# Kernel optimization log

Measured on AMD Instinct MI355X. Metric: run time of the kernel, lower is better.

The kernel has to match this reference:

```python
import jax, jax.numpy as jnp
import numpy as np
from jax import lax

# Model dims (match init_kwargs / input_specs)
B, T, N_IN, N_MID, N_OUT = 256, 100, 784, 1024, 10
L_TAU = 0.8  # state decay


def setup_inputs() -> dict:
    key = jax.random.key(0)
    ks = jax.random.split(key, 10)
    x = jax.random.uniform(ks[0], (B, T, N_IN), dtype=jnp.float32)  # input spikes/rates
    y = jax.random.randint(ks[1], (B,), 0, N_OUT, dtype=jnp.int64)

    def lin(k, fan_in, fan_out):
        return jax.random.normal(k, (fan_in, fan_out), dtype=jnp.float32) / np.sqrt(fan_in)

    return {
        "x": x, "y": y,
        "W1": lin(ks[2], N_IN, N_MID),  "b1": jnp.zeros((N_MID,), jnp.float32),
        "W2": lin(ks[3], N_MID, N_MID), "b2": jnp.zeros((N_MID,), jnp.float32),
        "W3": lin(ks[4], N_MID, N_MID), "b3": jnp.zeros((N_MID,), jnp.float32),
        "W4": lin(ks[5], N_MID, N_OUT), "b4": jnp.zeros((N_OUT,), jnp.float32),
    }


def _snu(s, y_prev, x_in, W, b):
    # SNU cell (soft): s_t = relu(W x_t + tau * s_{t-1} * (1 - y_{t-1})); y_t = sigmoid(s_t + b)
    s = jax.nn.relu(x_in @ W + L_TAU * s * (1.0 - y_prev))
    y_out = jax.nn.sigmoid(s + b)
    return s, y_out


def reference(x, y, W1, b1, W2, b2, W3, b3, W4, b4):
    bsz = x.shape[0]
    zeros = lambda n: jnp.zeros((bsz, n), x.dtype)
    carry0 = (zeros(N_MID), zeros(N_MID), zeros(N_MID), zeros(N_MID),
              zeros(N_MID), zeros(N_MID), zeros(N_OUT), zeros(N_OUT))

    def step(carry, x_t):
        s1, y1, s2, y2, s3, y3, s4, y4 = carry
        s1, y1 = _snu(s1, y1, x_t, W1, b1)
        s2, y2 = _snu(s2, y2, y1, W2, b2)
        s3, y3 = _snu(s3, y3, y2, W3, b3)
        s4, y4 = _snu(s4, y4, y3, W4, b4)
        return (s1, y1, s2, y2, s3, y3, s4, y4), y4

    xs = jnp.transpose(x, (1, 0, 2))  # [T, B, n_in]
    _, outs = lax.scan(step, carry0, xs)  # outs: [T, B, n_out]
    # out_rec also stacked the initial zero output; it contributes 0 to the sum
    m = jnp.sum(outs, axis=0)  # [B, n_out]
    logp = jax.nn.log_softmax(m, axis=-1)
    loss = -jnp.mean(jnp.take_along_axis(logp, y[:, None], axis=1))
    return loss, m
```

## Files before the change

kernel.cpp:

```cpp
#include <hip/hip_runtime.h>
#include <hip/hip_bf16.h>


#define BDIM 256
#define TT   100
#define BB   256
#define MM   25600
#define NMID 1024
#define K1   784
#define K1P  896
#define NOUT 10
#define N4P  16
#define L_TAU 0.8f

typedef __attribute__((ext_vector_type(4))) int   int4x;
typedef __attribute__((ext_vector_type(8))) int   int8x;
typedef __attribute__((ext_vector_type(4))) float f32x4;

__device__ __forceinline__ void async_copy16(const void* g, void* l) {
    __builtin_amdgcn_global_load_lds(
        (const __attribute__((address_space(1))) unsigned int*)g,
        (__attribute__((address_space(3))) unsigned int*)l,
        16, 0, 0);
}

__device__ __forceinline__ unsigned short f2bf(float f) {
    __hip_bfloat16 h = __float2bfloat16(f);
    return __builtin_bit_cast(unsigned short, h);
}
__device__ __forceinline__ float bf2f(unsigned short u) {
    return __uint_as_float((unsigned)u << 16);
}

__global__ void convert_x(const float* __restrict__ X, unsigned char* __restrict__ XB) {
    int m = blockIdx.x;
    int b = m & (BB - 1);
    int t = m >> 8;
    int th = threadIdx.x;
    if (th >= K1P / 4) return;
    int pk = 0;
    if (th < K1 / 4) {
        float4 v = *(const float4*)(X + ((long)b * TT + t) * K1 + th * 4);
        pk = __builtin_amdgcn_cvt_pk_fp8_f32(v.x, v.y, 0, false);
        pk = __builtin_amdgcn_cvt_pk_fp8_f32(v.z, v.w, pk, true);
    }
    *(int*)(XB + (long)m * K1P + th * 4) = pk;
}

__device__ __forceinline__ void tc_body(const float* __restrict__ W,
                                        unsigned char* __restrict__ WT,
                                        int K, int N, int Kpad,
                                        int bx, int by, int tidx) {
    __shared__ float tile[32][33];
    int k0 = bx * 32;
    int n0 = by * 32;
    int tx = tidx & 31, ty = tidx >> 5;
    #pragma unroll
    for (int i = 0; i < 4; ++i) {
        int k = k0 + ty + i * 8;
        tile[ty + i * 8][tx] = (k < K) ? W[(long)k * N + n0 + tx] : 0.0f;
    }
    __syncthreads();
    int nl = tidx >> 3, kq = tidx & 7;
    int pk = __builtin_amdgcn_cvt_pk_fp8_f32(tile[kq * 4 + 0][nl], tile[kq * 4 + 1][nl], 0, false);
    pk     = __builtin_amdgcn_cvt_pk_fp8_f32(tile[kq * 4 + 2][nl], tile[kq * 4 + 3][nl], pk, true);
    *(int*)(WT + (long)(n0 + nl) * Kpad + k0 + kq * 4) = pk;
}

__global__ void transpose_convert(const float* __restrict__ W, unsigned char* __restrict__ WT,
                                  int K, int N, int Kpad) {
    tc_body(W, WT, K, N, Kpad, blockIdx.x, blockIdx.y, threadIdx.x);
}

__global__ void transpose_convert2(const float* __restrict__ Wa, unsigned char* __restrict__ Ta,
                                   const float* __restrict__ Wb, unsigned char* __restrict__ Tb) {
    const float* W = blockIdx.z ? Wb : Wa;
    unsigned char* T = blockIdx.z ? Tb : Ta;
    tc_body(W, T, NMID, NMID, NMID, blockIdx.x, blockIdx.y, threadIdx.x);
}

__global__ void convert_w4(const float* __restrict__ W4, unsigned char* __restrict__ W4T) {
    int tid = blockIdx.x * BDIM + threadIdx.x;
    int n = tid >> 8;
    int k4 = (tid & 255) * 4;
    float v0 = 0, v1 = 0, v2 = 0, v3 = 0;
    if (n < NOUT) {
        v0 = W4[(k4 + 0) * NOUT + n];
        v1 = W4[(k4 + 1) * NOUT + n];
        v2 = W4[(k4 + 2) * NOUT + n];
        v3 = W4[(k4 + 3) * NOUT + n];
    }
    int pk = __builtin_amdgcn_cvt_pk_fp8_f32(v0, v1, 0, false);
    pk     = __builtin_amdgcn_cvt_pk_fp8_f32(v2, v3, pk, true);
    *(int*)(W4T + (long)n * NMID + k4) = pk;
}

#define BM 128
#define BN 128
#define BKB 128
#define MSTRIPS (MM / BM)
#define NSTRIPS (NMID / BN)
__global__ __launch_bounds__(256) void gemm_fp8(
    const unsigned char* __restrict__ A,
    const unsigned char* __restrict__ BT,
    __hip_bfloat16* __restrict__ C,
    int Kp)
{
    __shared__ unsigned char As[BM * BKB];
    __shared__ unsigned char Bs[BN * BKB];

    const int tid  = threadIdx.x;
    const int wave = tid >> 6;
    const int lane = tid & 63;

    const int l    = blockIdx.x;
    const int xcd  = l & 7;
    const int p    = l >> 3;
    const int bm   = (xcd * (MSTRIPS / 8) + (p >> 3)) * BM;
    const int bn   = (p & 7) * BN;

    const int wr = (wave >> 1) * 64;
    const int wc = (wave & 1) * 64;

    f32x4 acc[4][4] = {};

    const int srow = tid >> 3;
    const int lch  = tid & 7;
    const int gch  = lch ^ (srow & 7);
    const unsigned char* Aptr = A  + (long)(bm + srow) * Kp + gch * 16;
    const unsigned char* Bptr = BT + (long)(bn + srow) * Kp + gch * 16;

    for (int k0 = 0; k0 < Kp; k0 += BKB) {
        #pragma unroll
        for (int i = 0; i < 4; ++i) {
            async_copy16(Aptr + (long)(i * 32) * Kp + k0, &As[(srow + i * 32) * BKB + lch * 16]);
            async_copy16(Bptr + (long)(i * 32) * Kp + k0, &Bs[(srow + i * 32) * BKB + lch * 16]);
        }
        __syncthreads();

        const int mrow = lane & 15;
        const int g    = lane >> 4;
        int8x af[4], bfr[4];
        #pragma unroll
        for (int i = 0; i < 4; ++i) {
            int row = wr + i * 16 + mrow;
            int r7  = row & 7;
            int4x lo = *(const int4x*)&As[row * BKB + ((2 * g    ) ^ r7) * 16];
            int4x hi = *(const int4x*)&As[row * BKB + ((2 * g + 1) ^ r7) * 16];
            af[i][0] = lo[0]; af[i][1] = lo[1]; af[i][2] = lo[2]; af[i][3] = lo[3];
            af[i][4] = hi[0]; af[i][5] = hi[1]; af[i][6] = hi[2]; af[i][7] = hi[3];
        }
        #pragma unroll
        for (int j = 0; j < 4; ++j) {
            int row = wc + j * 16 + mrow;
            int r7  = row & 7;
            int4x lo = *(const int4x*)&Bs[row * BKB + ((2 * g    ) ^ r7) * 16];
            int4x hi = *(const int4x*)&Bs[row * BKB + ((2 * g + 1) ^ r7) * 16];
            bfr[j][0] = lo[0]; bfr[j][1] = lo[1]; bfr[j][2] = lo[2]; bfr[j][3] = lo[3];
            bfr[j][4] = hi[0]; bfr[j][5] = hi[1]; bfr[j][6] = hi[2]; bfr[j][7] = hi[3];
        }
        #pragma unroll
        for (int i = 0; i < 4; ++i)
            #pragma unroll
            for (int j = 0; j < 4; ++j)
                acc[i][j] = __builtin_amdgcn_mfma_scale_f32_16x16x128_f8f6f4(
                    bfr[j], af[i], acc[i][j],
                    0, 0,
                    0, 0x7F,
                    0, 0x7F);
        __syncthreads();
    }

    const int mcol  = lane & 15;
    const int nrow4 = (lane >> 4) * 4;
    #pragma unroll
    for (int i = 0; i < 4; ++i)
        #pragma unroll
        for (int j = 0; j < 4; ++j) {
            int gm = bm + wr + i * 16 + mcol;
            int gn = bn + wc + j * 16 + nrow4;
            ushort4 pk;
            pk.x = f2bf(acc[i][j][0]);
            pk.y = f2bf(acc[i][j][1]);
            pk.z = f2bf(acc[i][j][2]);
            pk.w = f2bf(acc[i][j][3]);
            *(ushort4*)&C[(long)gm * NMID + gn] = pk;
        }
}

__global__ void snu_recur(const __hip_bfloat16* __restrict__ Z,
                          const float* __restrict__ bias,
                          unsigned char* __restrict__ Y) {
    int idx = blockIdx.x * BDIM + threadIdx.x;
    int n2 = (idx & (NMID / 2 - 1)) * 2;
    int b  = idx >> 9;
    float2 bv = *(const float2*)(bias + n2);
    float s0 = 0.0f, y0 = 0.0f, s1 = 0.0f, y1 = 0.0f;
    const long base = (long)b * NMID + n2;
    const long stride = (long)BB * NMID;
    for (int t0 = 0; t0 < TT; t0 += 4) {
        ushort2 zz[4];
        #pragma unroll
        for (int j = 0; j < 4; ++j)
            zz[j] = *(const ushort2*)(Z + base + (t0 + j) * stride);
        #pragma unroll
        for (int j = 0; j < 4; ++j) {
            float z0 = bf2f(zz[j].x), z1 = bf2f(zz[j].y);
            s0 = fmaxf(fmaf(L_TAU * s0, 1.0f - y0, z0), 0.0f);
            y0 = 1.0f / (1.0f + __expf(-(s0 + bv.x)));
            s1 = fmaxf(fmaf(L_TAU * s1, 1.0f - y1, z1), 0.0f);
            y1 = 1.0f / (1.0f + __expf(-(s1 + bv.y)));
            int pk = __builtin_amdgcn_cvt_pk_fp8_f32(y0, y1, 0, false);
            *(unsigned short*)(Y + base + (t0 + j) * stride) = (unsigned short)pk;
        }
    }
}

__global__ __launch_bounds__(256) void layer4_gemm(const unsigned char* __restrict__ Y3,
                                                   const unsigned char* __restrict__ W4T,
                                                   float* __restrict__ Z4) {
    const int tid  = threadIdx.x;
    const int wave = tid >> 6;
    const int lane = tid & 63;
    const int mrow = lane & 15;
    const int g    = lane >> 4;
    const int row  = blockIdx.x * 64 + wave * 16 + mrow;
    const unsigned char* ap = Y3  + (long)row  * NMID + g * 32;
    const unsigned char* wp = W4T + (long)mrow * NMID + g * 32;
    f32x4 acc = {};
    #pragma unroll
    for (int kt = 0; kt < 8; ++kt) {
        int4x alo = *(const int4x*)(ap + kt * 128);
        int4x ahi = *(const int4x*)(ap + kt * 128 + 16);
        int4x wlo = *(const int4x*)(wp + kt * 128);
        int4x whi = *(const int4x*)(wp + kt * 128 + 16);
        int8x af, bf;
        af[0] = alo[0]; af[1] = alo[1]; af[2] = alo[2]; af[3] = alo[3];
        af[4] = ahi[0]; af[5] = ahi[1]; af[6] = ahi[2]; af[7] = ahi[3];
        bf[0] = wlo[0]; bf[1] = wlo[1]; bf[2] = wlo[2]; bf[3] = wlo[3];
        bf[4] = whi[0]; bf[5] = whi[1]; bf[6] = whi[2]; bf[7] = whi[3];
        acc = __builtin_amdgcn_mfma_scale_f32_16x16x128_f8f6f4(
            bf, af, acc, 0, 0, 0, 0x7F, 0, 0x7F);
    }
    *(f32x4*)&Z4[(long)row * N4P + g * 4] = acc;
}

__global__ void snu4_recur(const float* __restrict__ Z4, const float* __restrict__ b4,
                           float* __restrict__ m_out) {
    int idx = blockIdx.x * BDIM + threadIdx.x;
    int n = idx & 15;
    int b = idx >> 4;
    if (n >= NOUT) return;
    float bv = b4[n];
    float s = 0.0f, y = 0.0f, msum = 0.0f;
    for (int t0 = 0; t0 < TT; t0 += 4) {
        float z[4];
        #pragma unroll
        for (int j = 0; j < 4; ++j)
            z[j] = Z4[((long)(t0 + j) * BB + b) * N4P + n];
        #pragma unroll
        for (int j = 0; j < 4; ++j) {
            s = fmaxf(fmaf(L_TAU * s, 1.0f - y, z[j]), 0.0f);
            y = 1.0f / (1.0f + __expf(-(s + bv)));
            msum += y;
        }
    }
    m_out[b * NOUT + n] = msum;
}

__global__ void loss_kernel(const float* __restrict__ m, const int* __restrict__ y,
                            float* __restrict__ out) {
    __shared__ float red[BDIM];
    int b = threadIdx.x;
    float v[NOUT];
    float mx = -1e30f;
    #pragma unroll
    for (int n = 0; n < NOUT; ++n) { v[n] = m[b * NOUT + n]; mx = fmaxf(mx, v[n]); }
    float se = 0.0f;
    #pragma unroll
    for (int n = 0; n < NOUT; ++n) se += __expf(v[n] - mx);
    float lse = mx + __logf(se);
    int lbl = y[b];
    float vy = 0.0f;
    #pragma unroll
    for (int n = 0; n < NOUT; ++n) if (n == lbl) vy = v[n];
    red[b] = -(vy - lse);
    __syncthreads();
    for (int off = 128; off; off >>= 1) {
        if (b < off) red[b] += red[b + off];
        __syncthreads();
    }
    if (b == 0) out[0] = red[0] / (float)BB;
}

extern "C" void kernel_launch(void* const* d_in, const int* in_sizes, int n_in,
                              void* d_out, int out_size, void* d_ws, size_t ws_size,
                              hipStream_t stream) {
    const float* x  = (const float*)d_in[0];
    const int*   y  = (const int*)  d_in[1];
    const float* W1 = (const float*)d_in[2];
    const float* b1 = (const float*)d_in[3];
    const float* W2 = (const float*)d_in[4];
    const float* b2 = (const float*)d_in[5];
    const float* W3 = (const float*)d_in[6];
    const float* b3 = (const float*)d_in[7];
    const float* W4 = (const float*)d_in[8];
    const float* b4 = (const float*)d_in[9];
    float* out = (float*)d_out;

    char* ws = (char*)d_ws;
    size_t off = 0;
    auto alloc = [&](size_t bytes) {
        char* p = ws + off;
        off = (off + bytes + 255) & ~(size_t)255;
        return (void*)p;
    };
    unsigned char*  XB  = (unsigned char*) alloc((size_t)MM * K1P);
    unsigned char*  W1T = (unsigned char*) alloc((size_t)NMID * K1P);
    unsigned char*  W2T = (unsigned char*) alloc((size_t)NMID * NMID);
    unsigned char*  W3T = (unsigned char*) alloc((size_t)NMID * NMID);
    unsigned char*  W4T = (unsigned char*) alloc((size_t)N4P * NMID);
    __hip_bfloat16* Z   = (__hip_bfloat16*)alloc((size_t)MM * NMID * 2);
    unsigned char*  Ya  = (unsigned char*) alloc((size_t)MM * NMID);
    unsigned char*  Yb  = (unsigned char*) alloc((size_t)MM * NMID);
    float*          Z4  = (float*)         alloc((size_t)MM * N4P * 4);

    convert_x<<<MM, BDIM, 0, stream>>>(x, XB);
    transpose_convert<<<dim3(K1P / 32, NMID / 32), BDIM, 0, stream>>>(W1, W1T, K1, NMID, K1P);
    transpose_convert2<<<dim3(NMID / 32, NMID / 32, 2), BDIM, 0, stream>>>(W2, W2T, W3, W3T);
    convert_w4<<<N4P * NMID / 4 / BDIM, BDIM, 0, stream>>>(W4, W4T);

    const int gblocks = MSTRIPS * NSTRIPS;
    const int rblocks = (BB * NMID / 2) / BDIM;
    gemm_fp8<<<gblocks, BDIM, 0, stream>>>(XB, W1T, Z, K1P);
    snu_recur<<<rblocks, BDIM, 0, stream>>>(Z, b1, Ya);
    gemm_fp8<<<gblocks, BDIM, 0, stream>>>(Ya, W2T, Z, NMID);
    snu_recur<<<rblocks, BDIM, 0, stream>>>(Z, b2, Yb);
    gemm_fp8<<<gblocks, BDIM, 0, stream>>>(Yb, W3T, Z, NMID);
    snu_recur<<<rblocks, BDIM, 0, stream>>>(Z, b3, Ya);
    layer4_gemm<<<MM / 64, BDIM, 0, stream>>>(Ya, W4T, Z4);
    snu4_recur<<<(BB * N4P) / BDIM, BDIM, 0, stream>>>(Z4, b4, out + 1);
    loss_kernel<<<1, BDIM, 0, stream>>>(out + 1, y, out);
}
```

Baseline: 366.6 us.

## Fuse SNU recurrence into GEMM epilogue with batch-major padded time layout

```diff
diff --git a/kernel.cpp b/kernel.cpp
--- a/kernel.cpp
+++ b/kernel.cpp
@@ -4,8 +4,9 @@
 
 #define BDIM 256
 #define TT   100
+#define TP   112
 #define BB   256
-#define MM   25600
+#define MM2  (BB * TP)
 #define NMID 1024
 #define K1   784
 #define K1P  896
@@ -44,7 +45,7 @@
         pk = __builtin_amdgcn_cvt_pk_fp8_f32(v.x, v.y, 0, false);
         pk = __builtin_amdgcn_cvt_pk_fp8_f32(v.z, v.w, pk, true);
     }
-    *(int*)(XB + (long)m * K1P + th * 4) = pk;
+    *(int*)(XB + ((long)b * TP + t) * K1P + th * 4) = pk;
 }
 
 __device__ __forceinline__ void tc_body(const float* __restrict__ W,
@@ -95,123 +96,107 @@
     *(int*)(W4T + (long)n * NMID + k4) = pk;
 }
 
-#define BM 128
-#define BN 128
-#define BKB 128
-#define MSTRIPS (MM / BM)
-#define NSTRIPS (NMID / BN)
-__global__ __launch_bounds__(256) void gemm_fp8(
+__global__ __launch_bounds__(256) void gemm_snu_fused(
     const unsigned char* __restrict__ A,
     const unsigned char* __restrict__ BT,
-    __hip_bfloat16* __restrict__ C,
+    const float* __restrict__ bias,
+    unsigned char* __restrict__ Y,
     int Kp)
 {
-    __shared__ unsigned char As[BM * BKB];
-    __shared__ unsigned char Bs[BN * BKB];
+    __shared__ unsigned char smem[30720];
+    unsigned char* As = smem;
+    unsigned char* Bs = smem + 14336;
+    unsigned short* Zs = (unsigned short*)smem;
 
     const int tid  = threadIdx.x;
     const int wave = tid >> 6;
     const int lane = tid & 63;
 
-    const int l    = blockIdx.x;
-    const int xcd  = l & 7;
-    const int p    = l >> 3;
-    const int bm   = (xcd * (MSTRIPS / 8) + (p >> 3)) * BM;
-    const int bn   = (p & 7) * BN;
-
-    const int wr = (wave >> 1) * 64;
-    const int wc = (wave & 1) * 64;
-
-    f32x4 acc[4][4] = {};
+    const int l   = blockIdx.x;
+    const int xcd = l & 7;
+    const int p   = l >> 3;
+    const int b   = xcd * 32 + (p >> 3);
+    const int bn  = (p & 7) * 128;
+
+    const long arow0 = (long)b * TP;
+
+    f32x4 acc[7][2] = {};
 
     const int srow = tid >> 3;
     const int lch  = tid & 7;
     const int gch  = lch ^ (srow & 7);
-    const unsigned char* Aptr = A  + (long)(bm + srow) * Kp + gch * 16;
+    const unsigned char* Aptr = A  + (arow0 + srow) * Kp + gch * 16;
     const unsigned char* Bptr = BT + (long)(bn + srow) * Kp + gch * 16;
 
-    for (int k0 = 0; k0 < Kp; k0 += BKB) {
+    const int mrow = lane & 15;
+    const int g    = lane >> 4;
+    const int wc   = wave * 32;
+
+    for (int k0 = 0; k0 < Kp; k0 += 128) {
         #pragma unroll
         for (int i = 0; i < 4; ++i) {
-            async_copy16(Aptr + (long)(i * 32) * Kp + k0, &As[(srow + i * 32) * BKB + lch * 16]);
-            async_copy16(Bptr + (long)(i * 32) * Kp + k0, &Bs[(srow + i * 32) * BKB + lch * 16]);
+            if (srow + i * 32 < TP)
+                async_copy16(Aptr + (long)(i * 32) * Kp + k0,
+                             &As[(srow + i * 32) * 128 + lch * 16]);
+            async_copy16(Bptr + (long)(i * 32) * Kp + k0,
+                         &Bs[(srow + i * 32) * 128 + lch * 16]);
         }
         __syncthreads();
 
-        const int mrow = lane & 15;
-        const int g    = lane >> 4;
-        int8x af[4], bfr[4];
-        #pragma unroll
-        for (int i = 0; i < 4; ++i) {
-            int row = wr + i * 16 + mrow;
-            int r7  = row & 7;
-            int4x lo = *(const int4x*)&As[row * BKB + ((2 * g    ) ^ r7) * 16];
-            int4x hi = *(const int4x*)&As[row * BKB + ((2 * g + 1) ^ r7) * 16];
-            af[i][0] = lo[0]; af[i][1] = lo[1]; af[i][2] = lo[2]; af[i][3] = lo[3];
-            af[i][4] = hi[0]; af[i][5] = hi[1]; af[i][6] = hi[2]; af[i][7] = hi[3];
-        }
-        #pragma unroll
-        for (int j = 0; j < 4; ++j) {
+        int8x bfr[2];
+        #pragma unroll
+        for (int j = 0; j < 2; ++j) {
             int row = wc + j * 16 + mrow;
             int r7  = row & 7;
-            int4x lo = *(const int4x*)&Bs[row * BKB + ((2 * g    ) ^ r7) * 16];
-            int4x hi = *(const int4x*)&Bs[row * BKB + ((2 * g + 1) ^ r7) * 16];
+            int4x lo = *(const int4x*)&Bs[row * 128 + ((2 * g    ) ^ r7) * 16];
+            int4x hi = *(const int4x*)&Bs[row * 128 + ((2 * g + 1) ^ r7) * 16];
             bfr[j][0] = lo[0]; bfr[j][1] = lo[1]; bfr[j][2] = lo[2]; bfr[j][3] = lo[3];
             bfr[j][4] = hi[0]; bfr[j][5] = hi[1]; bfr[j][6] = hi[2]; bfr[j][7] = hi[3];
         }
         #pragma unroll
-        for (int i = 0; i < 4; ++i)
+        for (int i = 0; i < 7; ++i) {
+            int row = i * 16 + mrow;
+            int r7  = row & 7;
+            int4x lo = *(const int4x*)&As[row * 128 + ((2 * g    ) ^ r7) * 16];
+            int4x hi = *(const int4x*)&As[row * 128 + ((2 * g + 1) ^ r7) * 16];
+            int8x af;
+            af[0] = lo[0]; af[1] = lo[1]; af[2] = lo[2]; af[3] = lo[3];
+            af[4] = hi[0]; af[5] = hi[1]; af[6] = hi[2]; af[7] = hi[3];
             #pragma unroll
-            for (int j = 0; j < 4; ++j)
+            for (int j = 0; j < 2; ++j)
                 acc[i][j] = __builtin_amdgcn_mfma_scale_f32_16x16x128_f8f6f4(
-                    bfr[j], af[i], acc[i][j],
+                    bfr[j], af, acc[i][j],
                     0, 0,
                     0, 0x7F,
                     0, 0x7F);
+        }
         __syncthreads();
     }
 
-    const int mcol  = lane & 15;
-    const int nrow4 = (lane >> 4) * 4;
-    #pragma unroll
-    for (int i = 0; i < 4; ++i)
-        #pragma unroll
-        for (int j = 0; j < 4; ++j) {
-            int gm = bm + wr + i * 16 + mcol;
-            int gn = bn + wc + j * 16 + nrow4;
-            ushort4 pk;
-            pk.x = f2bf(acc[i][j][0]);
-            pk.y = f2bf(acc[i][j][1]);
-            pk.z = f2bf(acc[i][j][2]);
-            pk.w = f2bf(acc[i][j][3]);
-            *(ushort4*)&C[(long)gm * NMID + gn] = pk;
-        }
-}
-
-__global__ void snu_recur(const __hip_bfloat16* __restrict__ Z,
-                          const float* __restrict__ bias,
-                          unsigned char* __restrict__ Y) {
-    int idx = blockIdx.x * BDIM + threadIdx.x;
-    int n2 = (idx & (NMID / 2 - 1)) * 2;
-    int b  = idx >> 9;
-    float2 bv = *(const float2*)(bias + n2);
-    float s0 = 0.0f, y0 = 0.0f, s1 = 0.0f, y1 = 0.0f;
-    const long base = (long)b * NMID + n2;
-    const long stride = (long)BB * NMID;
-    for (int t0 = 0; t0 < TT; t0 += 4) {
-        ushort2 zz[4];
-        #pragma unroll
-        for (int j = 0; j < 4; ++j)
-            zz[j] = *(const ushort2*)(Z + base + (t0 + j) * stride);
-        #pragma unroll
-        for (int j = 0; j < 4; ++j) {
-            float z0 = bf2f(zz[j].x), z1 = bf2f(zz[j].y);
-            s0 = fmaxf(fmaf(L_TAU * s0, 1.0f - y0, z0), 0.0f);
-            y0 = 1.0f / (1.0f + __expf(-(s0 + bv.x)));
-            s1 = fmaxf(fmaf(L_TAU * s1, 1.0f - y1, z1), 0.0f);
-            y1 = 1.0f / (1.0f + __expf(-(s1 + bv.y)));
-            int pk = __builtin_amdgcn_cvt_pk_fp8_f32(y0, y1, 0, false);
-            *(unsigned short*)(Y + base + (t0 + j) * stride) = (unsigned short)pk;
+    #pragma unroll
+    for (int i = 0; i < 7; ++i)
+        #pragma unroll
+        for (int j = 0; j < 2; ++j) {
+            int t  = i * 16 + mrow;
+            int nn = wc + j * 16 + g * 4;
+            #pragma unroll
+            for (int r = 0; r < 4; ++r)
+                Zs[(nn + r) * 114 + t] = f2bf(acc[i][j][r]);
+        }
+    __syncthreads();
+
+    if (tid < 128) {
+        int n = tid;
+        float bv = bias[bn + n];
+        float s = 0.0f, yv = 0.0f;
+        const unsigned short* zp = Zs + n * 114;
+        unsigned char* yp = Y + arow0 * NMID + bn + n;
+        for (int t = 0; t < TT; ++t) {
+            float z = bf2f(zp[t]);
+            s = fmaxf(fmaf(L_TAU * s, 1.0f - yv, z), 0.0f);
+            yv = 1.0f / (1.0f + __expf(-(s + bv)));
+            int pk = __builtin_amdgcn_cvt_pk_fp8_f32(yv, yv, 0, false);
+            yp[(long)t * NMID] = (unsigned char)(pk & 0xFF);
         }
     }
 }
@@ -253,11 +238,12 @@
     if (n >= NOUT) return;
     float bv = b4[n];
     float s = 0.0f, y = 0.0f, msum = 0.0f;
+    const float* zp = Z4 + (long)b * TP * N4P + n;
     for (int t0 = 0; t0 < TT; t0 += 4) {
         float z[4];
         #pragma unroll
         for (int j = 0; j < 4; ++j)
-            z[j] = Z4[((long)(t0 + j) * BB + b) * N4P + n];
+            z[j] = zp[(t0 + j) * N4P];
         #pragma unroll
         for (int j = 0; j < 4; ++j) {
             s = fmaxf(fmaf(L_TAU * s, 1.0f - y, z[j]), 0.0f);
@@ -315,30 +301,25 @@
         off = (off + bytes + 255) & ~(size_t)255;
         return (void*)p;
     };
-    unsigned char*  XB  = (unsigned char*) alloc((size_t)MM * K1P);
-    unsigned char*  W1T = (unsigned char*) alloc((size_t)NMID * K1P);
-    unsigned char*  W2T = (unsigned char*) alloc((size_t)NMID * NMID);
-    unsigned char*  W3T = (unsigned char*) alloc((size_t)NMID * NMID);
-    unsigned char*  W4T = (unsigned char*) alloc((size_t)N4P * NMID);
-    __hip_bfloat16* Z   = (__hip_bfloat16*)alloc((size_t)MM * NMID * 2);
-    unsigned char*  Ya  = (unsigned char*) alloc((size_t)MM * NMID);
-    unsigned char*  Yb  = (unsigned char*) alloc((size_t)MM * NMID);
-    float*          Z4  = (float*)         alloc((size_t)MM * N4P * 4);
-
-    convert_x<<<MM, BDIM, 0, stream>>>(x, XB);
+    unsigned char* XB  = (unsigned char*)alloc((size_t)MM2 * K1P);
+    unsigned char* W1T = (unsigned char*)alloc((size_t)NMID * K1P);
+    unsigned char* W2T = (unsigned char*)alloc((size_t)NMID * NMID);
+    unsigned char* W3T = (unsigned char*)alloc((size_t)NMID * NMID);
+    unsigned char* W4T = (unsigned char*)alloc((size_t)N4P * NMID);
+    unsigned char* Ya  = (unsigned char*)alloc((size_t)MM2 * NMID);
+    unsigned char* Yb  = (unsigned char*)alloc((size_t)MM2 * NMID);
+    float*         Z4  = (float*)        alloc((size_t)MM2 * N4P * 4);
+
+    convert_x<<<BB * TT, BDIM, 0, stream>>>(x, XB);
     transpose_convert<<<dim3(K1P / 32, NMID / 32), BDIM, 0, stream>>>(W1, W1T, K1, NMID, K1P);
     transpose_convert2<<<dim3(NMID / 32, NMID / 32, 2), BDIM, 0, stream>>>(W2, W2T, W3, W3T);
     convert_w4<<<N4P * NMID / 4 / BDIM, BDIM, 0, stream>>>(W4, W4T);
 
-    const int gblocks = MSTRIPS * NSTRIPS;
-    const int rblocks = (BB * NMID / 2) / BDIM;
-    gemm_fp8<<<gblocks, BDIM, 0, stream>>>(XB, W1T, Z, K1P);
-    snu_recur<<<rblocks, BDIM, 0, stream>>>(Z, b1, Ya);
-    gemm_fp8<<<gblocks, BDIM, 0, stream>>>(Ya, W2T, Z, NMID);
-    snu_recur<<<rblocks, BDIM, 0, stream>>>(Z, b2, Yb);
-    gemm_fp8<<<gblocks, BDIM, 0, stream>>>(Yb, W3T, Z, NMID);
-    snu_recur<<<rblocks, BDIM, 0, stream>>>(Z, b3, Ya);
-    layer4_gemm<<<MM / 64, BDIM, 0, stream>>>(Ya, W4T, Z4);
+    const int fblocks = BB * (NMID / 128);
+    gemm_snu_fused<<<fblocks, BDIM, 0, stream>>>(XB, W1T, b1, Ya, K1P);
+    gemm_snu_fused<<<fblocks, BDIM, 0, stream>>>(Ya, W2T, b2, Yb, NMID);
+    gemm_snu_fused<<<fblocks, BDIM, 0, stream>>>(Yb, W3T, b3, Ya, NMID);
+    layer4_gemm<<<MM2 / 64, BDIM, 0, stream>>>(Ya, W4T, Z4);
     snu4_recur<<<(BB * N4P) / BDIM, BDIM, 0, stream>>>(Z4, b4, out + 1);
     loss_kernel<<<1, BDIM, 0, stream>>>(out + 1, y, out);
 }
```

Result: faster. 359.0 us (-2.1%).
